# Kernel optimization log

Hardware: AMD Instinct MI355X
Metric: run time of the kernel (lower is better)

Reference implementation:

```python
import jax, jax.numpy as jnp
import numpy as np

N, E, F_IN, H, C, G = 100000, 1600000, 128, 128, 10, 64


def setup_inputs() -> dict:
    key = jax.random.key(0)
    ks = jax.random.split(key, 9)
    x = jax.random.normal(ks[0], (N, F_IN), dtype=jnp.float32)
    edge_index = jax.random.randint(ks[1], (2, E), 0, N, dtype=jnp.int32)
    batch = jnp.sort(jax.random.randint(ks[2], (N,), 0, G, dtype=jnp.int32))
    s_in = 1.0 / np.sqrt(F_IN)
    s_h = 1.0 / np.sqrt(H)
    W1 = jax.random.normal(ks[3], (F_IN, H), jnp.float32) * s_in
    b1 = jnp.zeros((H,), jnp.float32)
    W2 = jax.random.normal(ks[4], (H, H), jnp.float32) * s_h
    b2 = jnp.zeros((H,), jnp.float32)
    Wfc = jax.random.normal(ks[5], (H, C), jnp.float32) * s_h
    bfc = jnp.zeros((C,), jnp.float32)
    return {"x": x, "edge_index": edge_index, "batch": batch,
            "W1": W1, "b1": b1, "W2": W2, "b2": b2, "Wfc": Wfc, "bfc": bfc}


def _gcn_conv(x, W, b, src, dst, n):
    # GCNConv: xW, symmetric deg^-1/2 normalization with self-loops, scatter-add, +bias
    xw = x @ W  # [N, H]
    deg = jnp.zeros((n,), xw.dtype).at[dst].add(1.0)  # in-degree incl. self-loop
    dis = jax.lax.rsqrt(jnp.maximum(deg, 1.0))
    norm = dis[src] * dis[dst]  # [E+N]
    out = jnp.zeros_like(xw).at[dst].add(xw[src] * norm[:, None])
    return out + b


def reference(x, edge_index, batch, W1, b1, W2, b2, Wfc, bfc):
    n = x.shape[0]
    loop = jnp.arange(n, dtype=edge_index.dtype)  # self-loops
    src = jnp.concatenate([edge_index[0], loop])
    dst = jnp.concatenate([edge_index[1], loop])
    h = jax.nn.relu(_gcn_conv(x, W1, b1, src, dst, n))
    h = jax.nn.relu(_gcn_conv(h, W2, b2, src, dst, n))
    # global mean pool over graph ids
    sums = jax.ops.segment_sum(h, batch, num_segments=G)  # [G, H]
    cnt = jax.ops.segment_sum(jnp.ones((n, 1), h.dtype), batch, num_segments=G)
    pooled = sums / jnp.maximum(cnt, 1.0)
    return pooled @ Wfc + bfc  # [G, C]
```

## Files before the change

kernel.cpp:

```cpp
#include <hip/hip_runtime.h>
#include <hip/hip_bf16.h>

#define NN 100000
#define NE 1600000
#define HD 128
#define NG 64
#define NC 10
#define NB 391
#define BCAP 4608
#define CHUNK 6400

typedef short bf16x8 __attribute__((ext_vector_type(8)));
typedef float f32x4 __attribute__((ext_vector_type(4)));

__device__ __forceinline__ unsigned pk_bf16(float a, float b) {
  unsigned ua = __float_as_uint(a);
  unsigned ub = __float_as_uint(b);
  unsigned ra = (ua + 0x7fffu + ((ua >> 16) & 1u)) >> 16;
  unsigned rb = (ub + 0x7fffu + ((ub >> 16) & 1u)) >> 16;
  return ra | (rb << 16);
}

#define ACC_U4(v)                                  \
  do {                                             \
    a0 += __uint_as_float((v).x << 16);            \
    a1 += __uint_as_float((v).x & 0xffff0000u);    \
    a2 += __uint_as_float((v).y << 16);            \
    a3 += __uint_as_float((v).y & 0xffff0000u);    \
    a4 += __uint_as_float((v).z << 16);            \
    a5 += __uint_as_float((v).z & 0xffff0000u);    \
    a6 += __uint_as_float((v).w << 16);            \
    a7 += __uint_as_float((v).w & 0xffff0000u);    \
  } while (0)

__global__ __launch_bounds__(256) void k_bin2(const int* __restrict__ src, const int* __restrict__ dst,
                                              int* __restrict__ bcnt, unsigned* __restrict__ bkt) {
  __shared__ int cl[NB];
  __shared__ int cb[NB];
  int tid = threadIdx.x;
  int base_e = blockIdx.x * CHUNK;
  for (int i = tid; i < NB; i += 256) cl[i] = 0;
  __syncthreads();
  #pragma unroll 5
  for (int j = 0; j < CHUNK / 256; ++j) {
    int d = dst[base_e + j * 256 + tid];
    atomicAdd(&cl[d >> 8], 1);
  }
  __syncthreads();
  for (int i = tid; i < NB; i += 256) {
    cb[i] = atomicAdd(&bcnt[i], cl[i]);
    cl[i] = 0;
  }
  __syncthreads();
  #pragma unroll 5
  for (int j = 0; j < CHUNK / 256; ++j) {
    int e = base_e + j * 256 + tid;
    int s = src[e];
    int d = dst[e];
    int b = d >> 8;
    int p = atomicAdd(&cl[b], 1);
    int idx = cb[b] + p;
    if (idx < BCAP)
      bkt[(size_t)b * BCAP + idx] = (unsigned)s | ((unsigned)(d & 255) << 24);
  }
}

__global__ __launch_bounds__(256) void k_fill2(const unsigned* __restrict__ bkt,
                                               const int* __restrict__ bcnt,
                                               int* __restrict__ rows, int* __restrict__ rowe,
                                               float* __restrict__ dis, int* __restrict__ csr) {
  __shared__ unsigned eds[BCAP];
  __shared__ int sc[256];
  int b = blockIdx.x;
  int tid = threadIdx.x;
  int n = bcnt[b];
  if (n > BCAP) n = BCAP;
  const unsigned* mb = bkt + (size_t)b * BCAP;
  for (int i = tid; i < n; i += 256) eds[i] = mb[i];
  sc[tid] = 0;
  __syncthreads();
  for (int i = tid; i < n; i += 256) atomicAdd(&sc[eds[i] >> 24], 1);
  __syncthreads();
  int deg = sc[tid];
  for (int off = 1; off < 256; off <<= 1) {
    int v = (tid >= off) ? sc[tid - off] : 0;
    __syncthreads();
    sc[tid] += v;
    __syncthreads();
  }
  int excl = sc[tid] - deg;
  int node = b * 256 + tid;
  int cbase = b * BCAP;
  if (node < NN) {
    rows[node] = cbase + excl;
    rowe[node] = cbase + excl + deg;
    dis[node] = rsqrtf((float)(deg + 1));
  }
  __syncthreads();
  sc[tid] = excl;
  __syncthreads();
  for (int i = tid; i < n; i += 256) {
    unsigned v = eds[i];
    int p = atomicAdd(&sc[v >> 24], 1);
    csr[cbase + p] = (int)(v & 0xFFFFFFu);
  }
}

__global__ __launch_bounds__(256) void k_prepW(const float* __restrict__ W1, const float* __restrict__ W2,
                                               unsigned* __restrict__ WT1, unsigned* __restrict__ WT2) {
  int i = blockIdx.x * 256 + threadIdx.x;
  const float* W = (i < 8192) ? W1 : W2;
  unsigned* WT = (i < 8192) ? WT1 : WT2;
  int j = i & 8191;
  int n = j >> 6, kh = j & 63;
  WT[j] = pk_bf16(W[(2 * kh) * HD + n], W[(2 * kh + 1) * HD + n]);
}

template<bool BF16IN>
__global__ __launch_bounds__(256) void k_gemm_mfma(const void* __restrict__ Xin,
                                                   const unsigned* __restrict__ WT,
                                                   const float* __restrict__ dis,
                                                   unsigned* __restrict__ Y) {
  __shared__ char WL[128 * 256];
  __shared__ char XL[64 * 256];
  int t = threadIdx.x;
  int rowBase = blockIdx.x * 64;
  {
    const uint4* Wg = (const uint4*)WT;
    for (int i = t; i < 2048; i += 256) {
      int n = i >> 4, kq = i & 15;
      uint4 v = Wg[i];
      *(uint4*)(WL + ((n * 256 + kq * 16) ^ ((n & 7) << 4))) = v;
    }
  }
  if (BF16IN) {
    const uint4* Xg = (const uint4*)Xin;
    for (int i = t; i < 1024; i += 256) {
      int node = i >> 4, c = i & 15;
      int gn = rowBase + node; if (gn >= NN) gn = 0;
      uint4 v = Xg[(size_t)gn * 16 + c];
      *(uint4*)(XL + ((node * 256 + c * 16) ^ ((node & 7) << 4))) = v;
    }
  } else {
    const float4* Xg = (const float4*)Xin;
    for (int i = t; i < 1024; i += 256) {
      int node = i >> 4, c = i & 15;
      int gn = rowBase + node; if (gn >= NN) gn = 0;
      float4 a = Xg[(size_t)gn * 32 + c * 2];
      float4 b = Xg[(size_t)gn * 32 + c * 2 + 1];
      uint4 v;
      v.x = pk_bf16(a.x, a.y); v.y = pk_bf16(a.z, a.w);
      v.z = pk_bf16(b.x, b.y); v.w = pk_bf16(b.z, b.w);
      *(uint4*)(XL + ((node * 256 + c * 16) ^ ((node & 7) << 4))) = v;
    }
  }
  __syncthreads();
  int w = t >> 6, l = t & 63;
  int lr = l & 15, lh = l >> 4;
  int xnode = w * 16 + lr;
  bf16x8 bfrag[4];
  #pragma unroll
  for (int ks = 0; ks < 4; ++ks)
    bfrag[ks] = *(bf16x8*)(XL + ((xnode * 256 + (ks * 32 + lh * 8) * 2) ^ ((xnode & 7) << 4)));
  f32x4 acc[8];
  #pragma unroll
  for (int ct = 0; ct < 8; ++ct) acc[ct] = (f32x4){0.f, 0.f, 0.f, 0.f};
  #pragma unroll
  for (int ct = 0; ct < 8; ++ct) {
    int n = ct * 16 + lr;
    #pragma unroll
    for (int ks = 0; ks < 4; ++ks) {
      bf16x8 af = *(bf16x8*)(WL + ((n * 256 + (ks * 32 + lh * 8) * 2) ^ ((n & 7) << 4)));
      acc[ct] = __builtin_amdgcn_mfma_f32_16x16x32_bf16(af, bfrag[ks], acc[ct], 0, 0, 0);
    }
  }
  int gnode = rowBase + w * 16 + lr;
  if (gnode < NN) {
    float ds = dis[gnode];
    uint2* Yp = (uint2*)(Y + (size_t)gnode * 64);
    #pragma unroll
    for (int ct = 0; ct < 8; ++ct) {
      uint2 o;
      o.x = pk_bf16(acc[ct].x * ds, acc[ct].y * ds);
      o.y = pk_bf16(acc[ct].z * ds, acc[ct].w * ds);
      Yp[ct * 4 + lh] = o;
    }
  }
}

template<int MODE>
__global__ __launch_bounds__(256) void k_agg(const unsigned* __restrict__ Y, const int* __restrict__ rows,
                                             const int* __restrict__ rowe, const int* __restrict__ csr,
                                             const float* __restrict__ dis,
                                             const float* __restrict__ bias,
                                             void* __restrict__ OUT) {
  int node = __builtin_amdgcn_readfirstlane((blockIdx.x << 2) + (threadIdx.x >> 6));
  int lane = threadIdx.x & 63;
  int sub = lane >> 4, li = lane & 15;
  const uint4* Yv = (const uint4*)Y;
  float a0 = 0.f, a1 = 0.f, a2 = 0.f, a3 = 0.f, a4 = 0.f, a5 = 0.f, a6 = 0.f, a7 = 0.f;
  if (sub == 0) {
    uint4 sv = Yv[(size_t)node * 16 + li];
    ACC_U4(sv);
  }
  int i = rows[node] + sub, end = rowe[node];
  for (; i + 4 < end; i += 8) {
    int s0 = csr[i], s1 = csr[i + 4];
    uint4 v0 = Yv[(size_t)s0 * 16 + li];
    uint4 v1 = Yv[(size_t)s1 * 16 + li];
    ACC_U4(v0);
    ACC_U4(v1);
  }
  if (i < end) {
    uint4 v = Yv[(size_t)csr[i] * 16 + li];
    ACC_U4(v);
  }
  a0 += __shfl_xor(a0, 16, 64); a0 += __shfl_xor(a0, 32, 64);
  a1 += __shfl_xor(a1, 16, 64); a1 += __shfl_xor(a1, 32, 64);
  a2 += __shfl_xor(a2, 16, 64); a2 += __shfl_xor(a2, 32, 64);
  a3 += __shfl_xor(a3, 16, 64); a3 += __shfl_xor(a3, 32, 64);
  a4 += __shfl_xor(a4, 16, 64); a4 += __shfl_xor(a4, 32, 64);
  a5 += __shfl_xor(a5, 16, 64); a5 += __shfl_xor(a5, 32, 64);
  a6 += __shfl_xor(a6, 16, 64); a6 += __shfl_xor(a6, 32, 64);
  a7 += __shfl_xor(a7, 16, 64); a7 += __shfl_xor(a7, 32, 64);
  if (sub != 0) return;
  float di = dis[node];
  const float4* bp = (const float4*)bias;
  float4 b0 = bp[li * 2], b1 = bp[li * 2 + 1];
  float o0 = fmaxf(fmaf(di, a0, b0.x), 0.f);
  float o1 = fmaxf(fmaf(di, a1, b0.y), 0.f);
  float o2 = fmaxf(fmaf(di, a2, b0.z), 0.f);
  float o3 = fmaxf(fmaf(di, a3, b0.w), 0.f);
  float o4 = fmaxf(fmaf(di, a4, b1.x), 0.f);
  float o5 = fmaxf(fmaf(di, a5, b1.y), 0.f);
  float o6 = fmaxf(fmaf(di, a6, b1.z), 0.f);
  float o7 = fmaxf(fmaf(di, a7, b1.w), 0.f);
  if (MODE == 0) {
    uint4 pv;
    pv.x = pk_bf16(o0, o1);
    pv.y = pk_bf16(o2, o3);
    pv.z = pk_bf16(o4, o5);
    pv.w = pk_bf16(o6, o7);
    ((uint4*)OUT)[(size_t)node * 16 + li] = pv;
  } else {
    float4* Op = (float4*)OUT + (size_t)node * 32 + li * 2;
    Op[0] = make_float4(o0, o1, o2, o3);
    Op[1] = make_float4(o4, o5, o6, o7);
  }
}

__global__ __launch_bounds__(256) void k_bounds(const int* __restrict__ bat, int* __restrict__ sg,
                                                int* __restrict__ eg) {
  int i = blockIdx.x * 256 + threadIdx.x;
  if (i < NN) {
    int g = bat[i];
    if (i == 0 || bat[i - 1] != g) sg[g] = i;
    if (i == NN - 1 || bat[i + 1] != g) eg[g] = i + 1;
  }
}

__global__ __launch_bounds__(128) void k_pool(const float* __restrict__ Hf, const int* __restrict__ sg,
                                              const int* __restrict__ eg, float* __restrict__ sums) {
  int g = blockIdx.x >> 5;
  int sl = blockIdx.x & 31;
  int f = threadIdx.x;
  int s = sg[g], e = eg[g];
  float acc = 0.f;
  for (int n = s + sl; n < e; n += 32) acc += Hf[(size_t)n * HD + f];
  atomicAdd(&sums[g * HD + f], acc);
}

__global__ __launch_bounds__(640) void k_fc(const float* __restrict__ sums, const int* __restrict__ sg,
                                            const int* __restrict__ eg, const float* __restrict__ Wfc,
                                            const float* __restrict__ bfc, float* __restrict__ out) {
  int t = threadIdx.x;
  if (t >= NG * NC) return;
  int g = t / NC, c = t - g * NC;
  int cntn = eg[g] - sg[g];
  float inv = 1.0f / fmaxf((float)cntn, 1.0f);
  float acc = 0.f;
  for (int f = 0; f < HD; ++f) acc = fmaf(sums[g * HD + f], Wfc[f * NC + c], acc);
  out[t] = acc * inv + bfc[c];
}

extern "C" void kernel_launch(void* const* d_in, const int* in_sizes, int n_in,
                              void* d_out, int out_size, void* d_ws, size_t ws_size,
                              hipStream_t stream) {
  const float* x   = (const float*)d_in[0];
  const int*   ei  = (const int*)d_in[1];
  const int*   bat = (const int*)d_in[2];
  const float* W1  = (const float*)d_in[3];
  const float* b1  = (const float*)d_in[4];
  const float* W2  = (const float*)d_in[5];
  const float* b2  = (const float*)d_in[6];
  const float* Wfc = (const float*)d_in[7];
  const float* bfc = (const float*)d_in[8];
  float* out = (float*)d_out;
  const int* esrc = ei;
  const int* edst = ei + NE;

  char* p = (char*)d_ws;
  auto carve = [&](size_t bytes) { char* r = p; p += (bytes + 255) & ~(size_t)255; return r; };
  float* dis  = (float*)carve((size_t)NN * 4);
  int*   rows = (int*)carve((size_t)NN * 4);
  int*   rowe = (int*)carve((size_t)NN * 4);
  int*   bcnt = (int*)carve((size_t)NB * 4);
  int*   sg   = (int*)carve(NG * 4);
  int*   eg   = (int*)carve(NG * 4);
  float* sums = (float*)carve(NG * HD * 4);
  unsigned* WT1 = (unsigned*)carve(8192 * 4);
  unsigned* WT2 = (unsigned*)carve(8192 * 4);
  int*   csr  = (int*)carve((size_t)NB * BCAP * 4);
  unsigned* Y   = (unsigned*)carve((size_t)NN * 64 * 4);
  float* H2   = (float*)carve((size_t)NN * HD * 4);
  unsigned* H1b = (unsigned*)H2;
  unsigned* bkt = Y;

  hipMemsetAsync(bcnt, 0, (size_t)NB * 4, stream);
  hipMemsetAsync(sums, 0, NG * HD * 4, stream);
  hipMemsetAsync(sg, 0, NG * 4, stream);
  hipMemsetAsync(eg, 0, NG * 4, stream);

  k_bin2<<<NE / CHUNK, 256, 0, stream>>>(esrc, edst, bcnt, bkt);
  k_fill2<<<NB, 256, 0, stream>>>(bkt, bcnt, rows, rowe, dis, csr);
  k_prepW<<<64, 256, 0, stream>>>(W1, W2, WT1, WT2);
  k_bounds<<<(NN + 255) / 256, 256, 0, stream>>>(bat, sg, eg);

  int gblocks = (NN + 63) / 64;
  k_gemm_mfma<false><<<gblocks, 256, 0, stream>>>(x, WT1, dis, Y);
  k_agg<0><<<NN / 4, 256, 0, stream>>>(Y, rows, rowe, csr, dis, b1, H1b);
  k_gemm_mfma<true><<<gblocks, 256, 0, stream>>>(H1b, WT2, dis, Y);
  k_agg<1><<<NN / 4, 256, 0, stream>>>(Y, rows, rowe, csr, dis, b2, H2);

  k_pool<<<NG * 32, 128, 0, stream>>>(H2, sg, eg, sums);
  k_fc<<<1, 640, 0, stream>>>(sums, sg, eg, Wfc, bfc, out);
}
```

Measured before the change: 264.6 us.

## Store layer-2 output in bf16, merge setup kernels, rebalance aggregation loop

The second aggregation now writes bf16 instead of fp32, halving the H2 write and the pooling read, and the pool kernel unpacks bf16 pairs. The weight prep, graph-bounds and sums-zeroing work are merged into one k_misc launch, removing three memsets and one kernel launch. The aggregation splits each node's edge range into four contiguous quarters per sub-wave with 4-way unrolled gathers instead of interleaved stride-4 access. Rounding layer-2 activations to bf16 before pooling adds a small precision loss, and sg/eg are no longer zeroed, so graphs with no nodes would read garbage.

```diff
diff --git a/kernel.cpp b/kernel.cpp
--- a/kernel.cpp
+++ b/kernel.cpp
@@ -106,14 +106,28 @@
   }
 }
 
-__global__ __launch_bounds__(256) void k_prepW(const float* __restrict__ W1, const float* __restrict__ W2,
-                                               unsigned* __restrict__ WT1, unsigned* __restrict__ WT2) {
-  int i = blockIdx.x * 256 + threadIdx.x;
-  const float* W = (i < 8192) ? W1 : W2;
-  unsigned* WT = (i < 8192) ? WT1 : WT2;
-  int j = i & 8191;
-  int n = j >> 6, kh = j & 63;
-  WT[j] = pk_bf16(W[(2 * kh) * HD + n], W[(2 * kh + 1) * HD + n]);
+__global__ __launch_bounds__(256) void k_misc(const float* __restrict__ W1, const float* __restrict__ W2,
+                                              unsigned* __restrict__ WT1, unsigned* __restrict__ WT2,
+                                              const int* __restrict__ bat, int* __restrict__ sg,
+                                              int* __restrict__ eg, float* __restrict__ sums) {
+  int bid = blockIdx.x;
+  int tid = threadIdx.x;
+  if (bid < 64) {
+    int i = bid * 256 + tid;
+    const float* W = (i < 8192) ? W1 : W2;
+    unsigned* WT = (i < 8192) ? WT1 : WT2;
+    int j = i & 8191;
+    int n = j >> 6, kh = j & 63;
+    WT[j] = pk_bf16(W[(2 * kh) * HD + n], W[(2 * kh + 1) * HD + n]);
+    if (i < NG * HD) sums[i] = 0.f;
+  } else {
+    int i = (bid - 64) * 256 + tid;
+    if (i < NN) {
+      int g = bat[i];
+      if (i == 0 || bat[i - 1] != g) sg[g] = i;
+      if (i == NN - 1 || bat[i + 1] != g) eg[g] = i + 1;
+    }
+  }
 }
 
 template<bool BF16IN>
@@ -188,30 +202,35 @@
   }
 }
 
-template<int MODE>
 __global__ __launch_bounds__(256) void k_agg(const unsigned* __restrict__ Y, const int* __restrict__ rows,
                                              const int* __restrict__ rowe, const int* __restrict__ csr,
                                              const float* __restrict__ dis,
                                              const float* __restrict__ bias,
-                                             void* __restrict__ OUT) {
+                                             unsigned* __restrict__ OUT) {
   int node = __builtin_amdgcn_readfirstlane((blockIdx.x << 2) + (threadIdx.x >> 6));
   int lane = threadIdx.x & 63;
   int sub = lane >> 4, li = lane & 15;
   const uint4* Yv = (const uint4*)Y;
   float a0 = 0.f, a1 = 0.f, a2 = 0.f, a3 = 0.f, a4 = 0.f, a5 = 0.f, a6 = 0.f, a7 = 0.f;
+  int start = rows[node], len = rowe[node] - start;
   if (sub == 0) {
     uint4 sv = Yv[(size_t)node * 16 + li];
     ACC_U4(sv);
   }
-  int i = rows[node] + sub, end = rowe[node];
-  for (; i + 4 < end; i += 8) {
-    int s0 = csr[i], s1 = csr[i + 4];
+  int i = start + ((len * sub) >> 2);
+  int q1 = start + ((len * (sub + 1)) >> 2);
+  for (; i + 4 <= q1; i += 4) {
+    int s0 = csr[i], s1 = csr[i + 1], s2 = csr[i + 2], s3 = csr[i + 3];
     uint4 v0 = Yv[(size_t)s0 * 16 + li];
     uint4 v1 = Yv[(size_t)s1 * 16 + li];
+    uint4 v2 = Yv[(size_t)s2 * 16 + li];
+    uint4 v3 = Yv[(size_t)s3 * 16 + li];
     ACC_U4(v0);
     ACC_U4(v1);
-  }
-  if (i < end) {
+    ACC_U4(v2);
+    ACC_U4(v3);
+  }
+  for (; i < q1; ++i) {
     uint4 v = Yv[(size_t)csr[i] * 16 + li];
     ACC_U4(v);
   }
@@ -235,39 +254,29 @@
   float o5 = fmaxf(fmaf(di, a5, b1.y), 0.f);
   float o6 = fmaxf(fmaf(di, a6, b1.z), 0.f);
   float o7 = fmaxf(fmaf(di, a7, b1.w), 0.f);
-  if (MODE == 0) {
-    uint4 pv;
-    pv.x = pk_bf16(o0, o1);
-    pv.y = pk_bf16(o2, o3);
-    pv.z = pk_bf16(o4, o5);
-    pv.w = pk_bf16(o6, o7);
-    ((uint4*)OUT)[(size_t)node * 16 + li] = pv;
-  } else {
-    float4* Op = (float4*)OUT + (size_t)node * 32 + li * 2;
-    Op[0] = make_float4(o0, o1, o2, o3);
-    Op[1] = make_float4(o4, o5, o6, o7);
-  }
-}
-
-__global__ __launch_bounds__(256) void k_bounds(const int* __restrict__ bat, int* __restrict__ sg,
-                                                int* __restrict__ eg) {
-  int i = blockIdx.x * 256 + threadIdx.x;
-  if (i < NN) {
-    int g = bat[i];
-    if (i == 0 || bat[i - 1] != g) sg[g] = i;
-    if (i == NN - 1 || bat[i + 1] != g) eg[g] = i + 1;
-  }
-}
-
-__global__ __launch_bounds__(128) void k_pool(const float* __restrict__ Hf, const int* __restrict__ sg,
+  uint4 pv;
+  pv.x = pk_bf16(o0, o1);
+  pv.y = pk_bf16(o2, o3);
+  pv.z = pk_bf16(o4, o5);
+  pv.w = pk_bf16(o6, o7);
+  ((uint4*)OUT)[(size_t)node * 16 + li] = pv;
+}
+
+__global__ __launch_bounds__(256) void k_pool(const unsigned* __restrict__ Hb, const int* __restrict__ sg,
                                               const int* __restrict__ eg, float* __restrict__ sums) {
-  int g = blockIdx.x >> 5;
-  int sl = blockIdx.x & 31;
-  int f = threadIdx.x;
+  int g = blockIdx.x >> 3;
+  int sl = blockIdx.x & 7;
+  int slot = threadIdx.x >> 6;
+  int pl = threadIdx.x & 63;
   int s = sg[g], e = eg[g];
-  float acc = 0.f;
-  for (int n = s + sl; n < e; n += 32) acc += Hf[(size_t)n * HD + f];
-  atomicAdd(&sums[g * HD + f], acc);
+  float f0 = 0.f, f1 = 0.f;
+  for (int n = s + sl * 4 + slot; n < e; n += 32) {
+    unsigned v = Hb[(size_t)n * 64 + pl];
+    f0 += __uint_as_float(v << 16);
+    f1 += __uint_as_float(v & 0xffff0000u);
+  }
+  atomicAdd(&sums[g * HD + 2 * pl], f0);
+  atomicAdd(&sums[g * HD + 2 * pl + 1], f1);
 }
 
 __global__ __launch_bounds__(640) void k_fc(const float* __restrict__ sums, const int* __restrict__ sg,
@@ -312,26 +321,22 @@
   unsigned* WT2 = (unsigned*)carve(8192 * 4);
   int*   csr  = (int*)carve((size_t)NB * BCAP * 4);
   unsigned* Y   = (unsigned*)carve((size_t)NN * 64 * 4);
-  float* H2   = (float*)carve((size_t)NN * HD * 4);
-  unsigned* H1b = (unsigned*)H2;
+  unsigned* H1b = (unsigned*)carve((size_t)NN * 64 * 4);
   unsigned* bkt = Y;
+  unsigned* H2b = H1b;
 
   hipMemsetAsync(bcnt, 0, (size_t)NB * 4, stream);
-  hipMemsetAsync(sums, 0, NG * HD * 4, stream);
-  hipMemsetAsync(sg, 0, NG * 4, stream);
-  hipMemsetAsync(eg, 0, NG * 4, stream);
 
   k_bin2<<<NE / CHUNK, 256, 0, stream>>>(esrc, edst, bcnt, bkt);
   k_fill2<<<NB, 256, 0, stream>>>(bkt, bcnt, rows, rowe, dis, csr);
-  k_prepW<<<64, 256, 0, stream>>>(W1, W2, WT1, WT2);
-  k_bounds<<<(NN + 255) / 256, 256, 0, stream>>>(bat, sg, eg);
+  k_misc<<<64 + (NN + 255) / 256, 256, 0, stream>>>(W1, W2, WT1, WT2, bat, sg, eg, sums);
 
   int gblocks = (NN + 63) / 64;
   k_gemm_mfma<false><<<gblocks, 256, 0, stream>>>(x, WT1, dis, Y);
-  k_agg<0><<<NN / 4, 256, 0, stream>>>(Y, rows, rowe, csr, dis, b1, H1b);
+  k_agg<<<NN / 4, 256, 0, stream>>>(Y, rows, rowe, csr, dis, b1, H1b);
   k_gemm_mfma<true><<<gblocks, 256, 0, stream>>>(H1b, WT2, dis, Y);
-  k_agg<1><<<NN / 4, 256, 0, stream>>>(Y, rows, rowe, csr, dis, b2, H2);
-
-  k_pool<<<NG * 32, 128, 0, stream>>>(H2, sg, eg, sums);
+  k_agg<<<NN / 4, 256, 0, stream>>>(Y, rows, rowe, csr, dis, b2, H2b);
+
+  k_pool<<<NG * 8, 256, 0, stream>>>(H2b, sg, eg, sums);
   k_fc<<<1, 640, 0, stream>>>(sums, sg, eg, Wfc, bfc, out);
 }
```

Result: faster. 251.0 us (-5.2%).
